# Performance work log

Hardware: AMD Instinct MI355X
Metric: run time of the kernel (lower is better)

Reference implementation:

```python
import jax, jax.numpy as jnp
import numpy as np

B, A, C, M = 32, 8400, 80, 32
TOP_K, ALPHA, BETA, EPS = 13, 1.0, 6.0, 1e-9


def _boxes(key, shape):
    # valid xyxy boxes in a 640x640 image
    u = jax.random.uniform(key, shape, jnp.float32)
    xy = u[..., :2] * 640.0
    wh = u[..., 2:] * 128.0 + 2.0
    return jnp.concatenate([xy, xy + wh], axis=-1)


def setup_inputs() -> dict:
    key = jax.random.key(0)
    k = jax.random.split(key, 6)
    pd_scores = jax.random.uniform(k[0], (B, A, C), jnp.float32)
    pd_bboxes = _boxes(k[1], (B, A, 4))
    anc_points = jax.random.uniform(k[2], (A, 2), jnp.float32) * 640.0
    gt_labels = jax.random.randint(k[3], (B, M, 1), 0, C, jnp.int32)
    gt_bboxes = _boxes(k[4], (B, M, 4))
    mask_gt = (jax.random.uniform(k[5], (B, M, 1)) < 0.8).astype(jnp.float32)
    return {"pd_scores": pd_scores, "pd_bboxes": pd_bboxes, "anc_points": anc_points,
            "gt_labels": gt_labels, "gt_bboxes": gt_bboxes, "mask_gt": mask_gt}


def _assign(pd_scores, pd_bboxes, anc_points, gt_labels, gt_bboxes, mask_gt):
    b, a, nc = pd_scores.shape
    m = gt_bboxes.shape[1]
    dtype = pd_scores.dtype

    # --- candidate anchors inside each GT box: (B, M, A) ---
    lt, rb = gt_bboxes[..., :2], gt_bboxes[..., 2:]                  # (B,M,2)
    deltas = jnp.concatenate([anc_points[None, None] - lt[:, :, None],
                              rb[:, :, None] - anc_points[None, None]], axis=-1)  # (B,M,A,4)
    mask_in_gts = (deltas.min(-1) > EPS).astype(dtype)               # (B,M,A)
    gt_mask = (mask_in_gts * mask_gt) > 0                            # bool (B,M,A)

    # --- classification score of each anchor for its GT's class ---
    labels = gt_labels[..., 0].astype(jnp.int32)                     # (B,M)
    scores_tc = jnp.swapaxes(pd_scores, 1, 2)                        # (B,C,A)
    idx = jnp.broadcast_to(labels[:, :, None], (b, m, a))
    bbox_scores = jnp.take_along_axis(scores_tc, idx, axis=1)        # (B,M,A)
    bbox_scores = jnp.where(gt_mask, bbox_scores, 0.0)

    # --- pairwise IoU gt x pred: (B,M,A) ---
    lt_i = jnp.maximum(gt_bboxes[:, :, None, :2], pd_bboxes[:, None, :, :2])
    rb_i = jnp.minimum(gt_bboxes[:, :, None, 2:], pd_bboxes[:, None, :, 2:])
    wh = jnp.clip(rb_i - lt_i, 0.0)
    inter = wh[..., 0] * wh[..., 1]
    area_g = ((gt_bboxes[..., 2] - gt_bboxes[..., 0]) * (gt_bboxes[..., 3] - gt_bboxes[..., 1]))[:, :, None]
    area_p = ((pd_bboxes[..., 2] - pd_bboxes[..., 0]) * (pd_bboxes[..., 3] - pd_bboxes[..., 1]))[:, None, :]
    iou = inter / (area_g + area_p - inter + EPS)
    overlaps = jnp.clip(jnp.where(gt_mask, iou, 0.0), 0.0)

    align_metric = bbox_scores ** ALPHA * overlaps ** BETA           # (B,M,A)

    # --- top-k over anchors, dedup via scatter-add counts ---
    tk_vals, tk_idx = jax.lax.top_k(align_metric, TOP_K)             # (B,M,K)
    tk_mask = jnp.broadcast_to(mask_gt > 0, (b, m, TOP_K))
    tk_idx = jnp.where(tk_mask, tk_idx, 0)
    bi = jnp.arange(b)[:, None, None]
    mi = jnp.arange(m)[None, :, None]
    counts = jnp.zeros((b, m, a), jnp.int32).at[bi, mi, tk_idx].add(1)
    mask_top_k = jnp.where(counts > 1, 0, counts).astype(dtype)

    mask_pos = mask_top_k * mask_in_gts * mask_gt                    # (B,M,A)
    fg_mask = mask_pos.sum(1)                                        # (B,A)

    # --- resolve anchors assigned to multiple GTs by max IoU ---
    # (always applied; identical to torch's conditional branch when no conflicts)
    mask_multi = jnp.broadcast_to(fg_mask[:, None, :] > 1, (b, m, a))
    max_ov_idx = jnp.argmax(overlaps, axis=1)                        # (B,A)
    is_max = (max_ov_idx[:, None, :] == jnp.arange(m)[None, :, None]).astype(dtype)
    mask_pos = jnp.where(mask_multi, is_max, mask_pos)
    fg_mask = mask_pos.sum(1)

    # --- gather targets ---
    tgt_idx = jnp.argmax(mask_pos, axis=1)                           # (B,A)
    tgt_labels = jnp.clip(jnp.take_along_axis(labels, tgt_idx, axis=1), 0)  # (B,A)
    tgt_bboxes = jnp.take_along_axis(gt_bboxes, jnp.broadcast_to(tgt_idx[:, :, None], (b, a, 4)), axis=1)

    one_hot = (tgt_labels[..., None] == jnp.arange(nc)).astype(dtype)  # (B,A,C)
    target_scores = one_hot * (fg_mask > 0)[..., None].astype(dtype)

    # --- normalize scores by aligned metric ---
    am = align_metric * mask_pos
    pos_am = am.max(-1, keepdims=True)                               # (B,M,1)
    pos_ov = (overlaps * mask_pos).max(-1, keepdims=True)            # (B,M,1)
    norm = (am * pos_ov / (pos_am + EPS)).max(axis=1)[..., None]     # (B,A,1)
    target_scores = target_scores * norm

    return tgt_bboxes, target_scores, fg_mask > 0


def reference(pd_scores, pd_bboxes, anc_points, gt_labels, gt_bboxes, mask_gt):
    return _assign(pd_scores, pd_bboxes, anc_points, gt_labels, gt_bboxes, mask_gt)
```

## Files before the change

### kernel.cpp

```cpp
#include <hip/hip_runtime.h>

#define Bq 32
#define Aq 8400
#define Cq 80
#define Mq 32
#define TOPK 13
#define CAP 512
#define EPSq 1e-9f

__device__ __forceinline__ bool better(float v1, int i1, float v2, int i2) {
    return (v1 > v2) || ((v1 == v2) && (i1 < i2));
}

__device__ __forceinline__ float iou4(float4 g, float4 p, float garea) {
    float ix1 = fmaxf(g.x, p.x), iy1 = fmaxf(g.y, p.y);
    float ix2 = fminf(g.z, p.z), iy2 = fminf(g.w, p.w);
    float iw = fmaxf(ix2 - ix1, 0.f), ih = fmaxf(iy2 - iy1, 0.f);
    float inter = iw * ih;
    float parea = (p.z - p.x) * (p.w - p.y);
    return inter / (((garea + parea) - inter) + EPSq);
}

__device__ __forceinline__ float in_min4(float ax, float ay, float4 g) {
    return fminf(fminf(ax - g.x, ay - g.y), fminf(g.z - ax, g.w - ay));
}

__device__ __forceinline__ void ins13(float (&val)[TOPK], int (&idx)[TOPK], float al, int a) {
    if (better(al, a, val[TOPK - 1], idx[TOPK - 1])) {
        #pragma unroll
        for (int k = TOPK - 1; k >= 1; --k) {
            bool bk   = better(val[k],     idx[k],     al, a);
            bool bkm1 = better(val[k - 1], idx[k - 1], al, a);
            val[k] = bk ? val[k] : (bkm1 ? al : val[k - 1]);
            idx[k] = bk ? idx[k] : (bkm1 ? a  : idx[k - 1]);
        }
        bool b0 = better(val[0], idx[0], al, a);
        val[0] = b0 ? val[0] : al;
        idx[0] = b0 ? idx[0] : a;
    }
}

__global__ __launch_bounds__(256) void k_compact(
    const float* __restrict__ anc, const float* __restrict__ gt_bboxes,
    const float* __restrict__ mask_gt,
    int* __restrict__ cnt, int* __restrict__ lists)
{
    __shared__ float4 sgb[Mq];
    __shared__ int    smv[Mq];
    int t = threadIdx.x;
    int a = blockIdx.x * 256 + t;
    int b = blockIdx.y;
    if (t < Mq) {
        sgb[t] = ((const float4*)gt_bboxes)[b * Mq + t];
        smv[t] = (mask_gt[b * Mq + t] > 0.f) ? 1 : 0;
    }
    __syncthreads();

    bool live = (a < Aq);
    float2 ap = live ? ((const float2*)anc)[a] : make_float2(-1e9f, -1e9f);
    int lane = t & 63;

    for (int m = 0; m < Mq; ++m) {
        bool in = live && smv[m] && (in_min4(ap.x, ap.y, sgb[m]) > EPSq);
        unsigned long long bal = __ballot(in);
        if (bal == 0ull) continue;
        int rank = __popcll(bal & ((1ull << lane) - 1ull));
        int leader = __ffsll(bal) - 1;
        int base = 0;
        if (lane == leader) base = atomicAdd(&cnt[b * Mq + m], __popcll(bal));
        base = __shfl(base, leader);
        if (in) {
            int pos = base + rank;
            if (pos < CAP) lists[((size_t)b * Mq + m) * CAP + pos] = a;
        }
    }
}

__global__ __launch_bounds__(256) void k_seltop(
    const float* __restrict__ pd_scores, const float* __restrict__ pd_bboxes,
    const float* __restrict__ anc, const int* __restrict__ gt_labels,
    const float* __restrict__ gt_bboxes, const float* __restrict__ mask_gt,
    const int* __restrict__ cnt, const int* __restrict__ lists,
    unsigned int* __restrict__ posmask)
{
    int w = threadIdx.x >> 6, lane = threadIdx.x & 63;
    int m = blockIdx.x * 4 + w;
    int b = blockIdx.y;
    if (mask_gt[b * Mq + m] <= 0.f) return;

    int lbl = gt_labels[b * Mq + m];
    float4 gb = ((const float4*)gt_bboxes)[b * Mq + m];
    float garea = (gb.z - gb.x) * (gb.w - gb.y);

    float val[TOPK]; int idx[TOPK];
    #pragma unroll
    for (int k = 0; k < TOPK; k++) { val[k] = -1.f; idx[k] = 0x7fffffff; }

    {
        float2 apl = ((const float2*)anc)[lane];
        if (!(in_min4(apl.x, apl.y, gb) > EPSq)) ins13(val, idx, 0.f, lane);
    }

    int n = cnt[b * Mq + m]; n = n < CAP ? n : CAP;
    for (int e = lane; e < n; e += 64) {
        int a = lists[((size_t)b * Mq + m) * CAP + e];
        float4 pb = ((const float4*)pd_bboxes)[(size_t)b * Aq + a];
        float ov = fmaxf(iou4(gb, pb, garea), 0.f);
        float sc = pd_scores[((size_t)b * Aq + a) * Cq + lbl];
        float o2 = ov * ov;
        ins13(val, idx, sc * (o2 * o2 * o2), a);
    }

    int win_i = 0x7fffffff;
    #pragma unroll
    for (int r = 0; r < TOPK; ++r) {
        float bv = val[0]; int bi = idx[0];
        #pragma unroll
        for (int off = 1; off < 64; off <<= 1) {
            float ovv = __shfl_xor(bv, off);
            int   oii = __shfl_xor(bi, off);
            if (better(ovv, oii, bv, bi)) { bv = ovv; bi = oii; }
        }
        if (lane == r) win_i = bi;
        if (idx[0] == bi) {
            #pragma unroll
            for (int k = 0; k < TOPK - 1; ++k) { val[k] = val[k + 1]; idx[k] = idx[k + 1]; }
            val[TOPK - 1] = -1.f; idx[TOPK - 1] = 0x7fffffff;
        }
    }
    if (lane < TOPK && win_i < Aq) {
        float2 ap = ((const float2*)anc)[win_i];
        if (in_min4(ap.x, ap.y, gb) > EPSq) {
            atomicOr(&posmask[b * Aq + win_i], 1u << m);
        }
    }
}

__global__ __launch_bounds__(256) void k_resolve(
    const float* __restrict__ pd_scores, const float* __restrict__ pd_bboxes,
    const float* __restrict__ anc, const int* __restrict__ gt_labels,
    const float* __restrict__ gt_bboxes, const float* __restrict__ mask_gt,
    const unsigned int* __restrict__ posmask,
    unsigned int* __restrict__ finalmask,
    float* __restrict__ asel,
    unsigned int* __restrict__ pos_am, unsigned int* __restrict__ pos_ov,
    float* __restrict__ out_bboxes, float* __restrict__ out_fg)
{
    int a = blockIdx.x * 256 + threadIdx.x;
    int b = blockIdx.y;
    if (a >= Aq) return;

    unsigned int w = posmask[b * Aq + a];
    float4 pb = ((const float4*)pd_bboxes)[(size_t)b * Aq + a];
    float2 ap = ((const float2*)anc)[a];

    if (__popc(w) > 1) {
        float bv = -1.f; int bj = 0;
        for (int mm = 0; mm < Mq; mm++) {
            float4 g = ((const float4*)gt_bboxes)[b * Mq + mm];
            float ov = 0.f;
            if (in_min4(ap.x, ap.y, g) > EPSq && mask_gt[b * Mq + mm] > 0.f) {
                float garea = (g.z - g.x) * (g.w - g.y);
                ov = fmaxf(iou4(g, pb, garea), 0.f);
            }
            if (ov > bv) { bv = ov; bj = mm; }
        }
        w = 1u << bj;
    }
    finalmask[b * Aq + a] = w;

    int j = w ? (__ffs(w) - 1) : 0;
    float4 g = ((const float4*)gt_bboxes)[b * Mq + j];
    ((float4*)out_bboxes)[(size_t)b * Aq + a] = g;
    out_fg[b * Aq + a] = w ? 1.f : 0.f;

    if (w) {
        float al = 0.f, ov = 0.f;
        if (in_min4(ap.x, ap.y, g) > EPSq && mask_gt[b * Mq + j] > 0.f) {
            float garea = (g.z - g.x) * (g.w - g.y);
            ov = fmaxf(iou4(g, pb, garea), 0.f);
            float sc = pd_scores[((size_t)b * Aq + a) * Cq + gt_labels[b * Mq + j]];
            float o2 = ov * ov;
            al = sc * (o2 * o2 * o2);
        }
        asel[b * Aq + a] = al;
        atomicMax(&pos_am[b * Mq + j], __float_as_uint(al));
        atomicMax(&pos_ov[b * Mq + j], __float_as_uint(ov));
    }
}

__global__ __launch_bounds__(256) void k_scores(
    const int* __restrict__ gt_labels,
    const unsigned int* __restrict__ finalmask,
    const float* __restrict__ asel,
    const unsigned int* __restrict__ pos_am, const unsigned int* __restrict__ pos_ov,
    float* __restrict__ out_scores)
{
    int i4 = blockIdx.x * 256 + threadIdx.x;
    if (i4 >= Bq * Aq * Cq / 4) return;
    int i = i4 * 4;
    int c0 = i % Cq;
    int ba = i / Cq;
    unsigned int w = finalmask[ba];
    float4 o = make_float4(0.f, 0.f, 0.f, 0.f);
    if (w) {
        int b = ba / Aq;
        int j = __ffs(w) - 1;
        int lb = gt_labels[b * Mq + j];
        if (lb >= c0 && lb < c0 + 4) {
            float pam = __uint_as_float(pos_am[b * Mq + j]);
            float pov = __uint_as_float(pos_ov[b * Mq + j]);
            float nv = asel[ba] * pov / (pam + EPSq);
            o.x = (lb == c0    ) ? nv : 0.f;
            o.y = (lb == c0 + 1) ? nv : 0.f;
            o.z = (lb == c0 + 2) ? nv : 0.f;
            o.w = (lb == c0 + 3) ? nv : 0.f;
        }
    }
    ((float4*)out_scores)[i4] = o;
}

extern "C" void kernel_launch(void* const* d_in, const int* in_sizes, int n_in,
                              void* d_out, int out_size, void* d_ws, size_t ws_size,
                              hipStream_t stream) {
    const float* pd_scores = (const float*)d_in[0];
    const float* pd_bboxes = (const float*)d_in[1];
    const float* anc       = (const float*)d_in[2];
    const int*   gt_labels = (const int*)d_in[3];
    const float* gt_bboxes = (const float*)d_in[4];
    const float* mask_gt   = (const float*)d_in[5];

    float* out_bboxes = (float*)d_out;
    float* out_scores = out_bboxes + (size_t)Bq * Aq * 4;
    float* out_fg     = out_scores + (size_t)Bq * Aq * Cq;

    char* ws = (char*)d_ws;
    const size_t BA4 = (size_t)Bq * Aq * 4;
    const size_t BM4 = (size_t)Bq * Mq * 4;
    unsigned int* posmask   = (unsigned int*)ws;  ws += BA4;
    unsigned int* pos_am    = (unsigned int*)ws;  ws += BM4;
    unsigned int* pos_ov    = (unsigned int*)ws;  ws += BM4;
    int*          cnt       = (int*)ws;           ws += BM4;
    unsigned int* finalmask = (unsigned int*)ws;  ws += BA4;
    float*        asel      = (float*)ws;         ws += BA4;
    int*          lists     = (int*)ws;           ws += (size_t)Bq * Mq * CAP * 4;

    hipMemsetAsync(posmask, 0, BA4 + 3 * BM4, stream);

    k_compact<<<dim3((Aq + 255) / 256, Bq), 256, 0, stream>>>(
        anc, gt_bboxes, mask_gt, cnt, lists);

    k_seltop<<<dim3(Mq / 4, Bq), 256, 0, stream>>>(
        pd_scores, pd_bboxes, anc, gt_labels, gt_bboxes, mask_gt,
        cnt, lists, posmask);

    k_resolve<<<dim3((Aq + 255) / 256, Bq), 256, 0, stream>>>(
        pd_scores, pd_bboxes, anc, gt_labels, gt_bboxes, mask_gt,
        posmask, finalmask, asel, pos_am, pos_ov, out_bboxes, out_fg);

    k_scores<<<(Bq * Aq * Cq / 4 + 255) / 256, 256, 0, stream>>>(
        gt_labels, finalmask, asel, pos_am, pos_ov, out_scores);
}
```

Measured before the change: 205.0 us.

## Fuse anchor compaction and top-k into one per-GT block kernel, drop posmask

Merges the compaction and top-k selection kernels into a single kernel with one block per (batch, GT). Each block scans all anchors, compacts the in-box candidates into shared memory and computes their align metrics in parallel before one wave does the top-k. Winners are written as a small index list that the resolve kernel scatters into a shared-memory mask, replacing the global posmask and its atomics. Zeroing of pos_am/pos_ov moves into the kernel, removing the memset launch. The trade-off is that every block scans all 8400 anchors, so anchor reads are repeated per GT, and each resolve block reads the full winners list.

```diff
diff --git a/kernel.cpp b/kernel.cpp
--- a/kernel.cpp
+++ b/kernel.cpp
@@ -40,76 +40,73 @@
     }
 }
 
-__global__ __launch_bounds__(256) void k_compact(
-    const float* __restrict__ anc, const float* __restrict__ gt_bboxes,
-    const float* __restrict__ mask_gt,
-    int* __restrict__ cnt, int* __restrict__ lists)
-{
-    __shared__ float4 sgb[Mq];
-    __shared__ int    smv[Mq];
-    int t = threadIdx.x;
-    int a = blockIdx.x * 256 + t;
-    int b = blockIdx.y;
-    if (t < Mq) {
-        sgb[t] = ((const float4*)gt_bboxes)[b * Mq + t];
-        smv[t] = (mask_gt[b * Mq + t] > 0.f) ? 1 : 0;
-    }
-    __syncthreads();
-
-    bool live = (a < Aq);
-    float2 ap = live ? ((const float2*)anc)[a] : make_float2(-1e9f, -1e9f);
-    int lane = t & 63;
-
-    for (int m = 0; m < Mq; ++m) {
-        bool in = live && smv[m] && (in_min4(ap.x, ap.y, sgb[m]) > EPSq);
-        unsigned long long bal = __ballot(in);
-        if (bal == 0ull) continue;
-        int rank = __popcll(bal & ((1ull << lane) - 1ull));
-        int leader = __ffsll(bal) - 1;
-        int base = 0;
-        if (lane == leader) base = atomicAdd(&cnt[b * Mq + m], __popcll(bal));
-        base = __shfl(base, leader);
-        if (in) {
-            int pos = base + rank;
-            if (pos < CAP) lists[((size_t)b * Mq + m) * CAP + pos] = a;
-        }
-    }
-}
-
-__global__ __launch_bounds__(256) void k_seltop(
+__global__ __launch_bounds__(256) void k_build(
     const float* __restrict__ pd_scores, const float* __restrict__ pd_bboxes,
     const float* __restrict__ anc, const int* __restrict__ gt_labels,
     const float* __restrict__ gt_bboxes, const float* __restrict__ mask_gt,
-    const int* __restrict__ cnt, const int* __restrict__ lists,
-    unsigned int* __restrict__ posmask)
+    unsigned int* __restrict__ zero_region,
+    int* __restrict__ winners)
 {
-    int w = threadIdx.x >> 6, lane = threadIdx.x & 63;
-    int m = blockIdx.x * 4 + w;
-    int b = blockIdx.y;
-    if (mask_gt[b * Mq + m] <= 0.f) return;
-
-    int lbl = gt_labels[b * Mq + m];
+    int m = blockIdx.x, b = blockIdx.y;
+    int t = threadIdx.x, lane = t & 63;
+
+    int gid = (b * Mq + m) * 256 + t;
+    if (gid < 2 * Bq * Mq) zero_region[gid] = 0u;
+
+    __shared__ int   s_n;
+    __shared__ int   s_list[CAP];
+    __shared__ float s_val[CAP];
+
+    if (mask_gt[b * Mq + m] <= 0.f) {
+        if (t < TOPK) winners[(b * Mq + m) * TOPK + t] = -1;
+        return;
+    }
+
+    if (t == 0) s_n = 0;
+    __syncthreads();
+
     float4 gb = ((const float4*)gt_bboxes)[b * Mq + m];
     float garea = (gb.z - gb.x) * (gb.w - gb.y);
 
-    float val[TOPK]; int idx[TOPK];
-    #pragma unroll
-    for (int k = 0; k < TOPK; k++) { val[k] = -1.f; idx[k] = 0x7fffffff; }
-
-    {
-        float2 apl = ((const float2*)anc)[lane];
-        if (!(in_min4(apl.x, apl.y, gb) > EPSq)) ins13(val, idx, 0.f, lane);
-    }
-
-    int n = cnt[b * Mq + m]; n = n < CAP ? n : CAP;
-    for (int e = lane; e < n; e += 64) {
-        int a = lists[((size_t)b * Mq + m) * CAP + e];
+    for (int a = t; a < Aq; a += 256) {
+        float2 ap = ((const float2*)anc)[a];
+        bool in = in_min4(ap.x, ap.y, gb) > EPSq;
+        unsigned long long bal = __ballot(in);
+        if (bal) {
+            int rank = __popcll(bal & ((1ull << lane) - 1ull));
+            int leader = __ffsll(bal) - 1;
+            int base = 0;
+            if (lane == leader) base = atomicAdd(&s_n, (int)__popcll(bal));
+            base = __shfl(base, leader);
+            int pos = base + rank;
+            if (in && pos < CAP) s_list[pos] = a;
+        }
+    }
+    __syncthreads();
+
+    int n = s_n < CAP ? s_n : CAP;
+    int lbl = gt_labels[b * Mq + m];
+    for (int e = t; e < n; e += 256) {
+        int a = s_list[e];
         float4 pb = ((const float4*)pd_bboxes)[(size_t)b * Aq + a];
         float ov = fmaxf(iou4(gb, pb, garea), 0.f);
         float sc = pd_scores[((size_t)b * Aq + a) * Cq + lbl];
         float o2 = ov * ov;
-        ins13(val, idx, sc * (o2 * o2 * o2), a);
-    }
+        s_val[e] = sc * (o2 * o2 * o2);
+    }
+    __syncthreads();
+
+    if (t >= 64) return;
+
+    float val[TOPK]; int idx[TOPK];
+    #pragma unroll
+    for (int k = 0; k < TOPK; k++) { val[k] = -1.f; idx[k] = 0x7fffffff; }
+
+    {
+        float2 apl = ((const float2*)anc)[lane];
+        if (!(in_min4(apl.x, apl.y, gb) > EPSq)) ins13(val, idx, 0.f, lane);
+    }
+    for (int e = lane; e < n; e += 64) ins13(val, idx, s_val[e], s_list[e]);
 
     int win_i = 0x7fffffff;
     #pragma unroll
@@ -128,11 +125,13 @@
             val[TOPK - 1] = -1.f; idx[TOPK - 1] = 0x7fffffff;
         }
     }
-    if (lane < TOPK && win_i < Aq) {
-        float2 ap = ((const float2*)anc)[win_i];
-        if (in_min4(ap.x, ap.y, gb) > EPSq) {
-            atomicOr(&posmask[b * Aq + win_i], 1u << m);
-        }
+    if (lane < TOPK) {
+        int outv = -1;
+        if (win_i < Aq) {
+            float2 ap = ((const float2*)anc)[win_i];
+            if (in_min4(ap.x, ap.y, gb) > EPSq) outv = win_i;
+        }
+        winners[(b * Mq + m) * TOPK + lane] = outv;
     }
 }
 
@@ -140,18 +139,34 @@
     const float* __restrict__ pd_scores, const float* __restrict__ pd_bboxes,
     const float* __restrict__ anc, const int* __restrict__ gt_labels,
     const float* __restrict__ gt_bboxes, const float* __restrict__ mask_gt,
-    const unsigned int* __restrict__ posmask,
-    unsigned int* __restrict__ finalmask,
-    float* __restrict__ asel,
+    const int* __restrict__ winners,
+    unsigned int* __restrict__ finalmask, float* __restrict__ asel,
     unsigned int* __restrict__ pos_am, unsigned int* __restrict__ pos_ov,
     float* __restrict__ out_bboxes, float* __restrict__ out_fg)
 {
-    int a = blockIdx.x * 256 + threadIdx.x;
     int b = blockIdx.y;
+    int a0 = blockIdx.x * 256;
+    int t = threadIdx.x;
+
+    __shared__ unsigned int smask[256];
+    smask[t] = 0u;
+    __syncthreads();
+
+    for (int e = t; e < Mq * TOPK; e += 256) {
+        int a = winners[(size_t)b * Mq * TOPK + e];
+        if (a >= a0 && a < a0 + 256) {
+            int m = e / TOPK;
+            atomicOr(&smask[a - a0], 1u << m);
+        }
+    }
+    __syncthreads();
+
+    int a = a0 + t;
     if (a >= Aq) return;
-
-    unsigned int w = posmask[b * Aq + a];
-    float4 pb = ((const float4*)pd_bboxes)[(size_t)b * Aq + a];
+    size_t i = (size_t)b * Aq + a;
+
+    unsigned int w = smask[t];
+    float4 pb = ((const float4*)pd_bboxes)[i];
     float2 ap = ((const float2*)anc)[a];
 
     if (__popc(w) > 1) {
@@ -167,23 +182,23 @@
         }
         w = 1u << bj;
     }
-    finalmask[b * Aq + a] = w;
+    finalmask[i] = w;
 
     int j = w ? (__ffs(w) - 1) : 0;
     float4 g = ((const float4*)gt_bboxes)[b * Mq + j];
-    ((float4*)out_bboxes)[(size_t)b * Aq + a] = g;
-    out_fg[b * Aq + a] = w ? 1.f : 0.f;
+    ((float4*)out_bboxes)[i] = g;
+    out_fg[i] = w ? 1.f : 0.f;
 
     if (w) {
         float al = 0.f, ov = 0.f;
         if (in_min4(ap.x, ap.y, g) > EPSq && mask_gt[b * Mq + j] > 0.f) {
             float garea = (g.z - g.x) * (g.w - g.y);
             ov = fmaxf(iou4(g, pb, garea), 0.f);
-            float sc = pd_scores[((size_t)b * Aq + a) * Cq + gt_labels[b * Mq + j]];
+            float sc = pd_scores[i * Cq + gt_labels[b * Mq + j]];
             float o2 = ov * ov;
             al = sc * (o2 * o2 * o2);
         }
-        asel[b * Aq + a] = al;
+        asel[i] = al;
         atomicMax(&pos_am[b * Mq + j], __float_as_uint(al));
         atomicMax(&pos_ov[b * Mq + j], __float_as_uint(ov));
     }
@@ -237,26 +252,19 @@
     char* ws = (char*)d_ws;
     const size_t BA4 = (size_t)Bq * Aq * 4;
     const size_t BM4 = (size_t)Bq * Mq * 4;
-    unsigned int* posmask   = (unsigned int*)ws;  ws += BA4;
     unsigned int* pos_am    = (unsigned int*)ws;  ws += BM4;
     unsigned int* pos_ov    = (unsigned int*)ws;  ws += BM4;
-    int*          cnt       = (int*)ws;           ws += BM4;
     unsigned int* finalmask = (unsigned int*)ws;  ws += BA4;
     float*        asel      = (float*)ws;         ws += BA4;
-    int*          lists     = (int*)ws;           ws += (size_t)Bq * Mq * CAP * 4;
-
-    hipMemsetAsync(posmask, 0, BA4 + 3 * BM4, stream);
-
-    k_compact<<<dim3((Aq + 255) / 256, Bq), 256, 0, stream>>>(
-        anc, gt_bboxes, mask_gt, cnt, lists);
-
-    k_seltop<<<dim3(Mq / 4, Bq), 256, 0, stream>>>(
+    int*          winners   = (int*)ws;           ws += (size_t)Bq * Mq * TOPK * 4;
+
+    k_build<<<dim3(Mq, Bq), 256, 0, stream>>>(
         pd_scores, pd_bboxes, anc, gt_labels, gt_bboxes, mask_gt,
-        cnt, lists, posmask);
+        pos_am , winners);
 
     k_resolve<<<dim3((Aq + 255) / 256, Bq), 256, 0, stream>>>(
         pd_scores, pd_bboxes, anc, gt_labels, gt_bboxes, mask_gt,
-        posmask, finalmask, asel, pos_am, pos_ov, out_bboxes, out_fg);
+        winners, finalmask, asel, pos_am, pos_ov, out_bboxes, out_fg);
 
     k_scores<<<(Bq * Aq * Cq / 4 + 255) / 256, 256, 0, stream>>>(
         gt_labels, finalmask, asel, pos_am, pos_ov, out_scores);
```

Result: faster. 190.7 us (-7.0%).
